# Kernel tuning notes

Measured on AMD Instinct MI355X. Metric: run time of the kernel, lower is better.

## Reference

```python
import jax, jax.numpy as jnp
import numpy as np

N = 100000   # nodes
E = 1600000  # directed edges (avg degree 16)
IN = 256     # input feature dim


def _gcn_norm(src, dst, n):
    # PyG gcn_norm with unit edge weights: deg computed on destination,
    # norm = deg^{-1/2}[src] * deg^{-1/2}[dst]
    deg = jax.ops.segment_sum(jnp.ones_like(dst, jnp.float32), dst, num_segments=n)
    dinv = jnp.where(deg > 0, jax.lax.rsqrt(deg), 0.0)
    return dinv[src] * dinv[dst]


def _gcn_conv(x, W, b, src, dst, norm, n):
    h = x @ W                          # [N, out] dense transform first (PyG order)
    msg = norm[:, None] * h[src]       # gather + scale  [E+N, out]
    agg = jax.ops.segment_sum(msg, dst, num_segments=n)  # scatter-add
    return agg + b


def setup_inputs() -> dict:
    key = jax.random.key(0)
    ks = jax.random.split(key, 5)
    x = jax.random.normal(ks[0], (N, IN), jnp.float32)
    edge_index = jax.random.randint(ks[1], (2, E), 0, N, dtype=jnp.int32)
    W1 = jax.random.normal(ks[2], (IN, 64), jnp.float32) * (1.0 / np.sqrt(IN))
    b1 = jnp.zeros((64,), jnp.float32)
    W2 = jax.random.normal(ks[3], (64, 32), jnp.float32) * (1.0 / np.sqrt(64))
    b2 = jnp.zeros((32,), jnp.float32)
    Wlin = jax.random.normal(ks[4], (32, 1), jnp.float32) * (1.0 / np.sqrt(32))
    blin = jnp.zeros((1,), jnp.float32)
    return {"x": x, "edge_index": edge_index, "W1": W1, "b1": b1,
            "W2": W2, "b2": b2, "Wlin": Wlin, "blin": blin}


def reference(x, edge_index, W1, b1, W2, b2, Wlin, blin):
    n = x.shape[0]
    loops = jnp.arange(n, dtype=edge_index.dtype)  # add self-loops (GCNConv default)
    src = jnp.concatenate([edge_index[0], loops])
    dst = jnp.concatenate([edge_index[1], loops])
    norm = _gcn_norm(src, dst, n)                  # same for both layers
    h = jax.nn.relu(_gcn_conv(x, W1, b1, src, dst, norm, n))
    h = jax.nn.relu(_gcn_conv(h, W2, b2, src, dst, norm, n))
    return h @ Wlin + blin
```

## Files before the change

### kernel.cpp

```cpp
#include <hip/hip_runtime.h>
#include <hip/hip_fp16.h>
#include <math.h>


#define BSH  9
#define BCAP 12288

typedef _Float16 half8 __attribute__((ext_vector_type(8)));
typedef float floatx4 __attribute__((ext_vector_type(4)));

static __global__ __launch_bounds__(256) void k_wfrag(const float* __restrict__ W1,
                                                      _Float16* __restrict__ w1f) {
    int t = threadIdx.x;
    for (int idx = t; idx < 2048; idx += 256) {
        int kb = idx >> 8;
        int nt = (idx >> 6) & 3;
        int l  = idx & 63;
        int k0 = kb * 32 + ((l >> 4) << 3);
        int nn = nt * 16 + (l & 15);
        half8 b;
        #pragma unroll
        for (int j = 0; j < 8; ++j) b[j] = (_Float16)W1[(k0 + j) * 64 + nn];
        *(half8*)(w1f + (size_t)idx * 8) = b;
    }
}

static __global__ __launch_bounds__(256) void k_fat(const float* __restrict__ x,
                                                    const _Float16* __restrict__ w1f,
                                                    _Float16* __restrict__ h1f,
                                                    const int* __restrict__ src,
                                                    const int* __restrict__ dst,
                                                    int* __restrict__ bkt_cnt,
                                                    int* __restrict__ epack,
                                                    int n, int e, int nScat) {
    __shared__ alignas(16) char smem[32768];
    int t = threadIdx.x;

    if ((int)blockIdx.x < nScat) {
        int*           sp    = (int*)smem;
        unsigned char* sbkt  = (unsigned char*)(smem + 16384);
        int*           cnt   = (int*)(smem + 20480);
        int*           loff  = (int*)(smem + 21504);
        int*           lcur  = (int*)(smem + 22528);
        int*           gbase = (int*)(smem + 23552);
        int*           sh    = (int*)(smem + 24576);
        int cb = blockIdx.x * 4096;
        int cc = min(4096, e - cb);

        cnt[t] = 0;
        __syncthreads();
        int ep[16]; unsigned char eb[16];
        int nv = 0;
        #pragma unroll
        for (int k = 0; k < 16; ++k) {
            int i = cb + k * 256 + t;
            if (i < e) {
                int s = src[i], d = dst[i];
                int b = d >> BSH;
                ep[nv] = ((d & 511) << 17) | s;
                eb[nv] = (unsigned char)b;
                atomicAdd(&cnt[b], 1);
                ++nv;
            }
        }
        __syncthreads();
        int v = cnt[t];
        sh[t] = v;
        __syncthreads();
        for (int o = 1; o < 256; o <<= 1) {
            int u = (t >= o) ? sh[t - o] : 0;
            __syncthreads();
            sh[t] += u;
            __syncthreads();
        }
        loff[t] = sh[t] - v;
        lcur[t] = sh[t] - v;
        if (v > 0) gbase[t] = t * BCAP + atomicAdd(&bkt_cnt[t], v);
        __syncthreads();
        for (int k = 0; k < nv; ++k) {
            int b = eb[k];
            int p = atomicAdd(&lcur[b], 1);
            sp[p] = ep[k];
            sbkt[p] = (unsigned char)b;
        }
        __syncthreads();
        for (int i = t; i < cc; i += 256) {
            int b = sbkt[i];
            epack[gbase[b] + (i - loff[b])] = sp[i];
        }
    } else {
        _Float16* Wl = (_Float16*)smem;
        {
            const float4* s = (const float4*)w1f;
            float4* d = (float4*)smem;
            #pragma unroll
            for (int i = 0; i < 8; ++i) d[t + i * 256] = s[t + i * 256];
        }
        __syncthreads();

        int l = t & 63;
        int w = t >> 6;
        int r0 = (blockIdx.x - nScat) * 128 + w * 32;
        int kq = (l >> 4) << 3;
        int ra0 = r0 + (l & 15);
        int ra1 = ra0 + 16;
        ra0 = ra0 < n ? ra0 : n - 1;
        ra1 = ra1 < n ? ra1 : n - 1;
        const float* p0 = x + (size_t)ra0 * 256 + kq;
        const float* p1 = x + (size_t)ra1 * 256 + kq;

        floatx4 acc[2][4];
        #pragma unroll
        for (int mt = 0; mt < 2; ++mt)
            #pragma unroll
            for (int nt = 0; nt < 4; ++nt)
                acc[mt][nt] = (floatx4){0.f, 0.f, 0.f, 0.f};

        #pragma unroll
        for (int kb = 0; kb < 8; ++kb) {
            float4 u0 = *(const float4*)(p0 + kb * 32);
            float4 u1 = *(const float4*)(p0 + kb * 32 + 4);
            float4 v0 = *(const float4*)(p1 + kb * 32);
            float4 v1 = *(const float4*)(p1 + kb * 32 + 4);
            half8 a0, a1;
            a0[0] = (_Float16)u0.x; a0[1] = (_Float16)u0.y; a0[2] = (_Float16)u0.z; a0[3] = (_Float16)u0.w;
            a0[4] = (_Float16)u1.x; a0[5] = (_Float16)u1.y; a0[6] = (_Float16)u1.z; a0[7] = (_Float16)u1.w;
            a1[0] = (_Float16)v0.x; a1[1] = (_Float16)v0.y; a1[2] = (_Float16)v0.z; a1[3] = (_Float16)v0.w;
            a1[4] = (_Float16)v1.x; a1[5] = (_Float16)v1.y; a1[6] = (_Float16)v1.z; a1[7] = (_Float16)v1.w;
            #pragma unroll
            for (int nt = 0; nt < 4; ++nt) {
                half8 b = *(const half8*)(Wl + ((size_t)(kb * 4 + nt) * 64 + l) * 8);
                acc[0][nt] = __builtin_amdgcn_mfma_f32_16x16x32_f16(a0, b, acc[0][nt], 0, 0, 0);
                acc[1][nt] = __builtin_amdgcn_mfma_f32_16x16x32_f16(a1, b, acc[1][nt], 0, 0, 0);
            }
        }

        int quad = l >> 4;
        int col  = l & 15;
        #pragma unroll
        for (int mt = 0; mt < 2; ++mt) {
            #pragma unroll
            for (int r = 0; r < 4; ++r) {
                int rr = r0 + mt * 16 + quad * 4 + r;
                if (rr < n) {
                    _Float16* o = h1f + (size_t)rr * 64 + col;
                    #pragma unroll
                    for (int nt = 0; nt < 4; ++nt)
                        o[nt * 16] = (_Float16)acc[mt][nt][r];
                }
            }
        }
    }
}

static __global__ __launch_bounds__(512) void k_bfinal(const int* __restrict__ bkt_cnt,
                                                       const int* __restrict__ epack,
                                                       float* __restrict__ dinv,
                                                       int* __restrict__ offs,
                                                       int* __restrict__ csr_src, int n) {
    __shared__ int cnt[512], sh[512], lcur[512];
    int t = threadIdx.x;
    int base = blockIdx.x << BSH;
    int e0 = blockIdx.x * BCAP;
    int e1 = e0 + bkt_cnt[blockIdx.x];
    cnt[t] = 0;
    __syncthreads();
    for (int i = e0 + t; i < e1; i += 512) atomicAdd(&cnt[epack[i] >> 17], 1);
    __syncthreads();
    int v = cnt[t];
    if (base + t < n) dinv[base + t] = 1.0f / sqrtf((float)(v + 1));
    sh[t] = v;
    __syncthreads();
    for (int o = 1; o < 512; o <<= 1) {
        int u = (t >= o) ? sh[t - o] : 0;
        __syncthreads();
        sh[t] += u;
        __syncthreads();
    }
    int incl = sh[t];
    if (base + t < n) offs[base + t] = e0 + incl;
    lcur[t] = e0 + incl - v;
    __syncthreads();
    for (int i = e0 + t; i < e1; i += 512) {
        int p = epack[i];
        int d = p >> 17;
        int pos = atomicAdd(&lcur[d], 1);
        csr_src[pos] = p & 0x1FFFF;
    }
}

static __global__ __launch_bounds__(256) void k_agg1gemm2(const int* __restrict__ offs,
                                                          const int* __restrict__ csr_src,
                                                          const float* __restrict__ dinv,
                                                          const __half2* __restrict__ h1h,
                                                          const float* __restrict__ b1,
                                                          const float* __restrict__ W2,
                                                          __half* __restrict__ h2h, int n) {
    __shared__ float Wl[64 * 32];
    __shared__ float aggL[8][64];
    int t = threadIdx.x;
    *(float4*)(Wl + t * 4)        = *(const float4*)(W2 + t * 4);
    *(float4*)(Wl + t * 4 + 1024) = *(const float4*)(W2 + t * 4 + 1024);

    int li = t & 31;
    int ni = t >> 5;
    int node  = blockIdx.x * 8 + ni;
    int nodeC = node < n ? node : n - 1;
    int start = (nodeC & 511) ? offs[nodeC - 1] : (nodeC >> BSH) * BCAP;
    int end   = offs[nodeC];
    float dd  = dinv[nodeC];
    float2 hf = __half22float2(h1h[(size_t)nodeC * 32 + li]);
    float accx = dd * hf.x, accy = dd * hf.y;

    int j = start;
    for (; j + 3 < end; j += 4) {
        int s0 = csr_src[j], s1 = csr_src[j + 1], s2 = csr_src[j + 2], s3 = csr_src[j + 3];
        float w0 = dinv[s0], w1 = dinv[s1], w2 = dinv[s2], w3 = dinv[s3];
        float2 v0 = __half22float2(h1h[(size_t)s0 * 32 + li]);
        float2 v1 = __half22float2(h1h[(size_t)s1 * 32 + li]);
        float2 v2 = __half22float2(h1h[(size_t)s2 * 32 + li]);
        float2 v3 = __half22float2(h1h[(size_t)s3 * 32 + li]);
        accx += w0 * v0.x + w1 * v1.x + w2 * v2.x + w3 * v3.x;
        accy += w0 * v0.y + w1 * v1.y + w2 * v2.y + w3 * v3.y;
    }
    for (; j < end; ++j) {
        int s = csr_src[j];
        float w = dinv[s];
        float2 v = __half22float2(h1h[(size_t)s * 32 + li]);
        accx += w * v.x;
        accy += w * v.y;
    }
    float2 bb = ((const float2*)b1)[li];
    aggL[ni][2 * li + 0] = fmaxf(dd * accx + bb.x, 0.f);
    aggL[ni][2 * li + 1] = fmaxf(dd * accy + bb.y, 0.f);
    __syncthreads();

    if (node < n) {
        float s = 0.f;
        #pragma unroll
        for (int k = 0; k < 64; ++k) s += aggL[ni][k] * Wl[k * 32 + li];
        h2h[(size_t)node * 32 + li] = __float2half(s);
    }
}

static __global__ __launch_bounds__(256) void k_gather2f(const int* __restrict__ offs,
                                                         const int* __restrict__ csr_src,
                                                         const float* __restrict__ dinv,
                                                         const __half2* __restrict__ h2h,
                                                         const float* __restrict__ b2,
                                                         const float* __restrict__ Wlin,
                                                         const float* __restrict__ blin,
                                                         float* __restrict__ out, int n) {
    int g    = blockIdx.x * 256 + threadIdx.x;
    int node = g >> 4;
    if (node >= n) return;
    int li = g & 15;
    int start = (node & 511) ? offs[node - 1] : (node >> BSH) * BCAP;
    int end   = offs[node];
    float dd  = dinv[node];
    float2 hf = __half22float2(h2h[(size_t)node * 16 + li]);
    float accx = dd * hf.x, accy = dd * hf.y;

    int j = start;
    for (; j + 3 < end; j += 4) {
        int s0 = csr_src[j], s1 = csr_src[j + 1], s2 = csr_src[j + 2], s3 = csr_src[j + 3];
        float w0 = dinv[s0], w1 = dinv[s1], w2 = dinv[s2], w3 = dinv[s3];
        float2 v0 = __half22float2(h2h[(size_t)s0 * 16 + li]);
        float2 v1 = __half22float2(h2h[(size_t)s1 * 16 + li]);
        float2 v2 = __half22float2(h2h[(size_t)s2 * 16 + li]);
        float2 v3 = __half22float2(h2h[(size_t)s3 * 16 + li]);
        accx += w0 * v0.x + w1 * v1.x + w2 * v2.x + w3 * v3.x;
        accy += w0 * v0.y + w1 * v1.y + w2 * v2.y + w3 * v3.y;
    }
    for (; j < end; ++j) {
        int s = csr_src[j];
        float w = dinv[s];
        float2 v = __half22float2(h2h[(size_t)s * 16 + li]);
        accx += w * v.x;
        accy += w * v.y;
    }
    float2 bb = ((const float2*)b2)[li];
    float2 wl = ((const float2*)Wlin)[li];
    float val = fmaxf(dd * accx + bb.x, 0.f) * wl.x +
                fmaxf(dd * accy + bb.y, 0.f) * wl.y;
    #pragma unroll
    for (int m = 8; m >= 1; m >>= 1) val += __shfl_xor(val, m);
    if (li == 0) out[node] = val + blin[0];
}

extern "C" void kernel_launch(void* const* d_in, const int* in_sizes, int n_in,
                              void* d_out, int out_size, void* d_ws, size_t ws_size,
                              hipStream_t stream) {
    const float* x    = (const float*)d_in[0];
    const int*   ei   = (const int*)d_in[1];
    const float* W1   = (const float*)d_in[2];
    const float* b1   = (const float*)d_in[3];
    const float* W2   = (const float*)d_in[4];
    const float* b2   = (const float*)d_in[5];
    const float* Wlin = (const float*)d_in[6];
    const float* blin = (const float*)d_in[7];
    float* out = (float*)d_out;

    const int n = in_sizes[0] / 256;
    const int e = in_sizes[1] / 2;
    const int* src = ei;
    const int* dst = ei + e;
    const int nbkt  = (n + (1 << BSH) - 1) >> BSH;
    const int nScat = (e + 4095) / 4096;
    const int nGemm = (n + 127) / 128;

    char* wp = (char*)d_ws;
    __half2*  h1h = (__half2*)wp;
    _Float16* h1f = (_Float16*)wp;    wp += (size_t)n * 32 * 4;
    __half*   h2h = (__half*)wp;      wp += (size_t)n * 32 * 2;
    float*    dinv = (float*)wp;      wp += (size_t)n * 4;
    int*      offs = (int*)wp;        wp += (size_t)n * 4;
    int*      csr_src = (int*)wp;     wp += (size_t)nbkt * BCAP * 4;
    int*      epack = (int*)wp;       wp += (size_t)nbkt * BCAP * 4;
    int*      bkt_cnt = (int*)wp;     wp += 256 * 4;
    _Float16* w1f = (_Float16*)wp;

    dim3 B(256);
    hipMemsetAsync(bkt_cnt, 0, 256 * 4, stream);
    k_wfrag <<<1, B, 0, stream>>>(W1, w1f);
    k_fat   <<<nScat + nGemm, B, 0, stream>>>(x, w1f, h1f, src, dst, bkt_cnt, epack, n, e, nScat);
    k_bfinal<<<nbkt, 512, 0, stream>>>(bkt_cnt, epack, dinv, offs, csr_src, n);
    k_agg1gemm2<<<(n + 7) / 8, B, 0, stream>>>(offs, csr_src, dinv, h1h, b1, W2, h2h, n);
    k_gather2f <<<(n * 16 + 255) / 256, B, 0, stream>>>(offs, csr_src, dinv, (const __half2*)h2h,
                                                        b2, Wlin, blin, out, n);
}
```

Measured before the change: 294.9 us.

## Pack quantized source norm into CSR entries and prefetch GEMM inputs

Adds a pass that packs a 15-bit quantized dinv[src] into the upper bits of each CSR source index. Both aggregation kernels can then drop the dependent random dinv gather, and their edge loops unroll by 8 to keep more loads in flight. The first-layer GEMM software-prefetches the next k-block of x and gets a launch-bounds occupancy hint. The costs are an extra kernel launch plus a read/write pass over the CSR array, and some precision loss from quantizing the normalization weights.

Result: slower. 304.2 us (+3.2%).

```diff
diff --git a/kernel.cpp b/kernel.cpp
--- a/kernel.cpp
+++ b/kernel.cpp
@@ -25,14 +25,14 @@
     }
 }
 
-static __global__ __launch_bounds__(256) void k_fat(const float* __restrict__ x,
-                                                    const _Float16* __restrict__ w1f,
-                                                    _Float16* __restrict__ h1f,
-                                                    const int* __restrict__ src,
-                                                    const int* __restrict__ dst,
-                                                    int* __restrict__ bkt_cnt,
-                                                    int* __restrict__ epack,
-                                                    int n, int e, int nScat) {
+static __global__ __launch_bounds__(256, 4) void k_fat(const float* __restrict__ x,
+                                                       const _Float16* __restrict__ w1f,
+                                                       _Float16* __restrict__ h1f,
+                                                       const int* __restrict__ src,
+                                                       const int* __restrict__ dst,
+                                                       int* __restrict__ bkt_cnt,
+                                                       int* __restrict__ epack,
+                                                       int n, int e, int nScat) {
     __shared__ alignas(16) char smem[32768];
     int t = threadIdx.x;
 
@@ -116,23 +116,32 @@
             for (int nt = 0; nt < 4; ++nt)
                 acc[mt][nt] = (floatx4){0.f, 0.f, 0.f, 0.f};
 
+        float4 cu0 = *(const float4*)(p0);
+        float4 cu1 = *(const float4*)(p0 + 4);
+        float4 cv0 = *(const float4*)(p1);
+        float4 cv1 = *(const float4*)(p1 + 4);
+
         #pragma unroll
         for (int kb = 0; kb < 8; ++kb) {
-            float4 u0 = *(const float4*)(p0 + kb * 32);
-            float4 u1 = *(const float4*)(p0 + kb * 32 + 4);
-            float4 v0 = *(const float4*)(p1 + kb * 32);
-            float4 v1 = *(const float4*)(p1 + kb * 32 + 4);
+            float4 nu0, nu1, nv0, nv1;
+            if (kb < 7) {
+                nu0 = *(const float4*)(p0 + (kb + 1) * 32);
+                nu1 = *(const float4*)(p0 + (kb + 1) * 32 + 4);
+                nv0 = *(const float4*)(p1 + (kb + 1) * 32);
+                nv1 = *(const float4*)(p1 + (kb + 1) * 32 + 4);
+            }
             half8 a0, a1;
-            a0[0] = (_Float16)u0.x; a0[1] = (_Float16)u0.y; a0[2] = (_Float16)u0.z; a0[3] = (_Float16)u0.w;
-            a0[4] = (_Float16)u1.x; a0[5] = (_Float16)u1.y; a0[6] = (_Float16)u1.z; a0[7] = (_Float16)u1.w;
-            a1[0] = (_Float16)v0.x; a1[1] = (_Float16)v0.y; a1[2] = (_Float16)v0.z; a1[3] = (_Float16)v0.w;
-            a1[4] = (_Float16)v1.x; a1[5] = (_Float16)v1.y; a1[6] = (_Float16)v1.z; a1[7] = (_Float16)v1.w;
+            a0[0] = (_Float16)cu0.x; a0[1] = (_Float16)cu0.y; a0[2] = (_Float16)cu0.z; a0[3] = (_Float16)cu0.w;
+            a0[4] = (_Float16)cu1.x; a0[5] = (_Float16)cu1.y; a0[6] = (_Float16)cu1.z; a0[7] = (_Float16)cu1.w;
+            a1[0] = (_Float16)cv0.x; a1[1] = (_Float16)cv0.y; a1[2] = (_Float16)cv0.z; a1[3] = (_Float16)cv0.w;
+            a1[4] = (_Float16)cv1.x; a1[5] = (_Float16)cv1.y; a1[6] = (_Float16)cv1.z; a1[7] = (_Float16)cv1.w;
             #pragma unroll
             for (int nt = 0; nt < 4; ++nt) {
                 half8 b = *(const half8*)(Wl + ((size_t)(kb * 4 + nt) * 64 + l) * 8);
                 acc[0][nt] = __builtin_amdgcn_mfma_f32_16x16x32_f16(a0, b, acc[0][nt], 0, 0, 0);
                 acc[1][nt] = __builtin_amdgcn_mfma_f32_16x16x32_f16(a1, b, acc[1][nt], 0, 0, 0);
             }
+            cu0 = nu0; cu1 = nu1; cv0 = nv0; cv1 = nv1;
         }
 
         int quad = l >> 4;
@@ -186,6 +195,19 @@
         int d = p >> 17;
         int pos = atomicAdd(&lcur[d], 1);
         csr_src[pos] = p & 0x1FFFF;
+    }
+}
+
+static __global__ __launch_bounds__(512) void k_wpack(int* __restrict__ csr_src,
+                                                      const float* __restrict__ dinv,
+                                                      const int* __restrict__ bkt_cnt) {
+    int b  = blockIdx.x;
+    int e0 = b * BCAP;
+    int e1 = e0 + bkt_cnt[b];
+    for (int i = e0 + threadIdx.x; i < e1; i += 512) {
+        int s = csr_src[i];
+        int q = (int)(dinv[s] * 32767.0f + 0.5f);
+        csr_src[i] = s | (q << 17);
     }
 }
 
@@ -212,20 +234,26 @@
     float2 hf = __half22float2(h1h[(size_t)nodeC * 32 + li]);
     float accx = dd * hf.x, accy = dd * hf.y;
 
+    const float QS = 1.0f / 32767.0f;
     int j = start;
-    for (; j + 3 < end; j += 4) {
-        int s0 = csr_src[j], s1 = csr_src[j + 1], s2 = csr_src[j + 2], s3 = csr_src[j + 3];
-        float w0 = dinv[s0], w1 = dinv[s1], w2 = dinv[s2], w3 = dinv[s3];
-        float2 v0 = __half22float2(h1h[(size_t)s0 * 32 + li]);
-        float2 v1 = __half22float2(h1h[(size_t)s1 * 32 + li]);
-        float2 v2 = __half22float2(h1h[(size_t)s2 * 32 + li]);
-        float2 v3 = __half22float2(h1h[(size_t)s3 * 32 + li]);
-        accx += w0 * v0.x + w1 * v1.x + w2 * v2.x + w3 * v3.x;
-        accy += w0 * v0.y + w1 * v1.y + w2 * v2.y + w3 * v3.y;
+    for (; j + 7 < end; j += 8) {
+        int pk[8];
+        #pragma unroll
+        for (int u = 0; u < 8; ++u) pk[u] = csr_src[j + u];
+        float2 vv[8]; float wq[8];
+        #pragma unroll
+        for (int u = 0; u < 8; ++u) {
+            int s = pk[u] & 0x1FFFF;
+            wq[u] = (float)(((unsigned)pk[u]) >> 17) * QS;
+            vv[u] = __half22float2(h1h[(size_t)s * 32 + li]);
+        }
+        #pragma unroll
+        for (int u = 0; u < 8; ++u) { accx += wq[u] * vv[u].x; accy += wq[u] * vv[u].y; }
     }
     for (; j < end; ++j) {
-        int s = csr_src[j];
-        float w = dinv[s];
+        int p = csr_src[j];
+        int s = p & 0x1FFFF;
+        float w = (float)(((unsigned)p) >> 17) * QS;
         float2 v = __half22float2(h1h[(size_t)s * 32 + li]);
         accx += w * v.x;
         accy += w * v.y;
@@ -261,20 +289,26 @@
     float2 hf = __half22float2(h2h[(size_t)node * 16 + li]);
     float accx = dd * hf.x, accy = dd * hf.y;
 
+    const float QS = 1.0f / 32767.0f;
     int j = start;
-    for (; j + 3 < end; j += 4) {
-        int s0 = csr_src[j], s1 = csr_src[j + 1], s2 = csr_src[j + 2], s3 = csr_src[j + 3];
-        float w0 = dinv[s0], w1 = dinv[s1], w2 = dinv[s2], w3 = dinv[s3];
-        float2 v0 = __half22float2(h2h[(size_t)s0 * 16 + li]);
-        float2 v1 = __half22float2(h2h[(size_t)s1 * 16 + li]);
-        float2 v2 = __half22float2(h2h[(size_t)s2 * 16 + li]);
-        float2 v3 = __half22float2(h2h[(size_t)s3 * 16 + li]);
-        accx += w0 * v0.x + w1 * v1.x + w2 * v2.x + w3 * v3.x;
-        accy += w0 * v0.y + w1 * v1.y + w2 * v2.y + w3 * v3.y;
+    for (; j + 7 < end; j += 8) {
+        int pk[8];
+        #pragma unroll
+        for (int u = 0; u < 8; ++u) pk[u] = csr_src[j + u];
+        float2 vv[8]; float wq[8];
+        #pragma unroll
+        for (int u = 0; u < 8; ++u) {
+            int s = pk[u] & 0x1FFFF;
+            wq[u] = (float)(((unsigned)pk[u]) >> 17) * QS;
+            vv[u] = __half22float2(h2h[(size_t)s * 16 + li]);
+        }
+        #pragma unroll
+        for (int u = 0; u < 8; ++u) { accx += wq[u] * vv[u].x; accy += wq[u] * vv[u].y; }
     }
     for (; j < end; ++j) {
-        int s = csr_src[j];
-        float w = dinv[s];
+        int p = csr_src[j];
+        int s = p & 0x1FFFF;
+        float w = (float)(((unsigned)p) >> 17) * QS;
         float2 v = __half22float2(h2h[(size_t)s * 16 + li]);
         accx += w * v.x;
         accy += w * v.y;
@@ -325,6 +359,7 @@
     k_wfrag <<<1, B, 0, stream>>>(W1, w1f);
     k_fat   <<<nScat + nGemm, B, 0, stream>>>(x, w1f, h1f, src, dst, bkt_cnt, epack, n, e, nScat);
     k_bfinal<<<nbkt, 512, 0, stream>>>(bkt_cnt, epack, dinv, offs, csr_src, n);
+    k_wpack <<<nbkt, 512, 0, stream>>>(csr_src, dinv, bkt_cnt);
     k_agg1gemm2<<<(n + 7) / 8, B, 0, stream>>>(offs, csr_src, dinv, h1h, b1, W2, h2h, n);
     k_gather2f <<<(n * 16 + 255) / 256, B, 0, stream>>>(offs, csr_src, dinv, (const __half2*)h2h,
                                                         b2, Wlin, blin, out, n);
```
